# Kernel optimization log

Measured on AMD Instinct MI355X. Metric: run time of the kernel, lower is better.

## Reference

```python
import jax, jax.numpy as jnp
import numpy as np

# --- configuration constants (from conf) ---
FEAT_H, FEAT_W, STRIDE = 32, 110, 16       # KITTI 512x1760 image, stride 16
B, G, NA = 8, 32, 36                       # batch, max GT per image, anchors per location
NUM_CLASSES = 4                            # len(lbls)+1
FG_T, BG_LO, BG_HI, BEST_T = 0.5, 0.0, 0.5, 0.35
L_CLS, L_2D, L_3D = 1.0, 1.0, 1.0          # cls_2d_lambda, bbox_2d_lambda, bbox_3d_lambda


def _locate_anchors(anchors):
    """Tile anchor templates over the feature grid. Returns boxes [A,4], tracker [A]."""
    sx = (jnp.arange(FEAT_W) * STRIDE).astype(jnp.float32)
    sy = (jnp.arange(FEAT_H) * STRIDE).astype(jnp.float32)
    gx, gy = jnp.meshgrid(sx, sy)                              # [H,W]
    shifts = jnp.stack([gx, gy, gx, gy], -1).reshape(-1, 4)    # [H*W,4]
    boxes = shifts[:, None, :] + anchors[None, :, 0:4]         # [H*W,NA,4]
    tracker = jnp.broadcast_to(jnp.arange(NA), (FEAT_H * FEAT_W, NA))
    return boxes.reshape(-1, 4), tracker.reshape(-1)


def _iou(rois, gts):
    # rois [A,4], gts [G,4] -> IoU [A,G]
    x1 = jnp.maximum(rois[:, None, 0], gts[None, :, 0])
    y1 = jnp.maximum(rois[:, None, 1], gts[None, :, 1])
    x2 = jnp.minimum(rois[:, None, 2], gts[None, :, 2])
    y2 = jnp.minimum(rois[:, None, 3], gts[None, :, 3])
    iw = jnp.clip(x2 - x1 + 1.0, 0.0)
    ih = jnp.clip(y2 - y1 + 1.0, 0.0)
    inter = iw * ih
    ar = (rois[:, 2] - rois[:, 0] + 1.0) * (rois[:, 3] - rois[:, 1] + 1.0)
    ag = (gts[:, 2] - gts[:, 0] + 1.0) * (gts[:, 3] - gts[:, 1] + 1.0)
    return inter / (ar[:, None] + ag[None, :] - inter)


def _smooth_l1(x):
    ax = jnp.abs(x)
    return jnp.where(ax < 1.0, 0.5 * ax * ax, ax - 0.5)


def setup_inputs() -> dict:
    key = jax.random.key(0)
    ks = jax.random.split(key, 10)
    A = FEAT_H * FEAT_W * NA
    cls = jax.random.normal(ks[0], (B, A, NUM_CLASSES), jnp.float32)
    bbox_2d = jax.random.normal(ks[1], (B, A, 4), jnp.float32) * 0.1
    bbox_3d = jax.random.normal(ks[2], (B, A, 7), jnp.float32) * 0.1
    # GT 2D boxes inside a 512x1760 image
    x1 = jax.random.uniform(ks[3], (B, G)) * 1500.0
    y1 = jax.random.uniform(ks[4], (B, G)) * 350.0
    w = 30.0 + jax.random.uniform(ks[5], (B, G)) * 200.0
    h = 30.0 + jax.random.uniform(ks[6], (B, G)) * 130.0
    gt_boxes = jnp.stack([x1, y1, x1 + w - 1.0, y1 + h - 1.0], -1)
    # GT 3D: [cx_proj, cy_proj, z, w3d, h3d, l3d, ry]
    k7, k8, k9 = jax.random.split(ks[7], 3)
    z = 5.0 + jax.random.uniform(k7, (B, G)) * 55.0
    dims = 1.0 + jax.random.uniform(k8, (B, G, 3)) * 3.0
    ry = (jax.random.uniform(k9, (B, G)) - 0.5) * (2.0 * np.pi)
    gt_3d = jnp.concatenate([(x1 + w * 0.5)[..., None], (y1 + h * 0.5)[..., None],
                             z[..., None], dims, ry[..., None]], -1)
    gt_labels = jax.random.randint(ks[8], (B, G), 1, NUM_CLASSES)
    gt_valid = jnp.ones((B, G), bool)
    # anchors: [x1,y1,x2,y2, z, w3d, h3d, l3d, ry] (12 scales x 3 aspect ratios)
    scales = np.array([32.0 * (1.26 ** i) for i in range(12)], np.float32)
    ratios = np.array([0.5, 1.0, 1.5], np.float32)
    aw = np.repeat(scales, 3)
    ah = (scales[:, None] * ratios[None, :]).reshape(-1)
    az = np.linspace(60.0, 5.0, NA).astype(np.float32)
    box = np.stack([-(aw - 1) / 2, -(ah - 1) / 2, (aw - 1) / 2, (ah - 1) / 2], -1)
    a3 = np.tile(np.array([1.6, 1.5, 3.9, 0.0], np.float32), (NA, 1))
    anchors = jnp.asarray(np.concatenate([box, az[:, None], a3], -1), jnp.float32)
    bbox_means = jnp.zeros((1, 11), jnp.float32)
    bbox_stds = jnp.concatenate([jnp.full((1, 4), 0.1, jnp.float32),
                                 jnp.full((1, 7), 0.5, jnp.float32)], -1)
    return {"cls": cls, "bbox_2d": bbox_2d, "bbox_3d": bbox_3d,
            "gt_boxes": gt_boxes, "gt_3d": gt_3d, "gt_labels": gt_labels,
            "gt_valid": gt_valid, "anchors": anchors,
            "bbox_means": bbox_means, "bbox_stds": bbox_stds}


def reference(cls, bbox_2d, bbox_3d, gt_boxes, gt_3d, gt_labels, gt_valid,
              anchors, bbox_means, bbox_stds):
    roi_boxes, tracker = _locate_anchors(anchors)          # [A,4], [A]
    widths = roi_boxes[:, 2] - roi_boxes[:, 0] + 1.0
    heights = roi_boxes[:, 3] - roi_boxes[:, 1] + 1.0
    ctr_x = roi_boxes[:, 0] + 0.5 * widths
    ctr_y = roi_boxes[:, 1] + 0.5 * heights
    src = anchors[tracker]                                 # [A,9] per-roi anchor template
    Gn = gt_boxes.shape[1]

    def assign(gtb, gt3, glbl, gval):
        iou = _iou(roi_boxes, gtb)                         # [A,G]
        iou = jnp.where(gval[None, :], iou, -1.0)
        max_ol = iou.max(1)
        agt = iou.argmax(1)                                # assigned GT per anchor
        fg = max_ol >= FG_T
        # best-anchor-per-gt rule (best_thresh)
        gt_best = iou.max(0)
        ba = iou.argmax(0)
        force = gval & (gt_best >= BEST_T)
        fg = fg.at[ba].max(force)
        agt = agt.at[ba].set(jnp.where(force, jnp.arange(Gn), agt[ba]))
        bg = (~fg) & (max_ol < BG_HI) & (max_ol >= BG_LO)  # rest is ignored
        g = gtb[agt]
        g3 = gt3[agt]
        gw = g[:, 2] - g[:, 0] + 1.0
        gh = g[:, 3] - g[:, 1] + 1.0
        gcx = g[:, 0] + 0.5 * gw
        gcy = g[:, 1] + 0.5 * gh
        t2 = jnp.stack([(gcx - ctr_x) / widths, (gcy - ctr_y) / heights,
                        jnp.log(gw / widths), jnp.log(gh / heights)], -1)
        t3 = jnp.stack([(g3[:, 0] - ctr_x) / widths, (g3[:, 1] - ctr_y) / heights,
                        g3[:, 2] - src[:, 4],
                        jnp.log(g3[:, 3] / src[:, 5]),
                        jnp.log(g3[:, 4] / src[:, 6]),
                        jnp.log(g3[:, 5] / src[:, 7]),
                        g3[:, 6] - src[:, 8]], -1)
        t2 = (t2 - bbox_means[0, 0:4]) / bbox_stds[0, 0:4]
        t3 = (t3 - bbox_means[0, 4:11]) / bbox_stds[0, 4:11]
        lbl = jnp.where(fg, glbl[agt], 0)
        return lbl, fg, bg, t2, t3

    lbl, fg, bg, t2, t3 = jax.vmap(assign)(gt_boxes, gt_3d, gt_labels, gt_valid)
    lbl = jax.lax.stop_gradient(lbl)
    t2 = jax.lax.stop_gradient(t2)
    t3 = jax.lax.stop_gradient(t3)
    active = (fg | bg).astype(cls.dtype)
    fgf = fg.astype(cls.dtype)
    logp = jax.nn.log_softmax(cls, -1)
    ce = -jnp.take_along_axis(logp, lbl[..., None], -1)[..., 0]
    n_act = jnp.maximum(active.sum(), 1.0)
    n_fg = jnp.maximum(fgf.sum(), 1.0)
    loss_cls = (ce * active).sum() / n_act
    loss_2d = (_smooth_l1(bbox_2d - t2).sum(-1) * fgf).sum() / n_fg
    loss_3d = (_smooth_l1(bbox_3d - t3).sum(-1) * fgf).sum() / n_fg
    return L_CLS * loss_cls + L_2D * loss_2d + L_3D * loss_3d
```

## Files before the change

kernel.cpp:

```cpp
#include <hip/hip_runtime.h>

#define FEAT_H 32
#define FEAT_W 110
#define NCELL (FEAT_H * FEAT_W)
#define STRIDEPX 16
#define NB 8
#define NG 32
#define NANC 36
#define NC 4
#define A_TOTAL (NCELL * NANC)

#define CPB 576

#define BLK 512
#define CHK 512
#define NCHK 248
#define G2 512
#define CB (G2 / NB)
#define MAXSLOTS 4

__device__ __forceinline__ float smooth_l1(float x) {
    float ax = fabsf(x);
    return ax < 1.f ? 0.5f * ax * ax : ax - 0.5f;
}



__global__ __launch_bounds__(CPB) void k_colpass(
    const float* __restrict__ gt_boxes, const int* __restrict__ gt_valid,
    const float* __restrict__ anchors, unsigned long long* __restrict__ colpart,
    float* __restrict__ acc, unsigned* __restrict__ done) {
#pragma clang fp contract(off)
    __shared__ unsigned long long cand[NANC];
    const int tid = threadIdx.x;
    const int bg = blockIdx.x;
    if (bg == 0) {
        if (tid < 8) acc[tid] = 0.f;
        if (tid == 8) *done = 0u;
    }
    const int t = tid >> 4;
    const int lane = tid & 15;
    const int valid = gt_valid[bg];
    const float g0 = gt_boxes[bg * 4 + 0], g1 = gt_boxes[bg * 4 + 1];
    const float g2 = gt_boxes[bg * 4 + 2], g3 = gt_boxes[bg * 4 + 3];
    const float ag = (g2 - g0 + 1.f) * (g3 - g1 + 1.f);
    const float* ap = anchors + t * 9;
    const float ax0 = ap[0], ay0 = ap[1], ax1 = ap[2], ay1 = ap[3];
    const float aarea = (ax1 - ax0 + 1.f) * (ay1 - ay0 + 1.f);

    float iwm = -1.f; int icol = 0;
    for (int col = lane; col < FEAT_W; col += 16) {
        const float sx = (float)(col * STRIDEPX);
        const float r0 = sx + ax0, r2 = sx + ax1;
        const float xx1 = fmaxf(r0, g0), xx2 = fminf(r2, g2);
        const float iw = fmaxf(xx2 - xx1 + 1.f, 0.f);
        if (iw > iwm) { iwm = iw; icol = col; }
    }
    float ihm = -1.f; int irow = 0;
    for (int row = lane; row < FEAT_H; row += 16) {
        const float sy = (float)(row * STRIDEPX);
        const float r1 = sy + ay0, r3 = sy + ay1;
        const float yy1 = fmaxf(r1, g1), yy2 = fminf(r3, g3);
        const float ih = fmaxf(yy2 - yy1 + 1.f, 0.f);
        if (ih > ihm) { ihm = ih; irow = row; }
    }
    for (int off = 8; off; off >>= 1) {
        const float ow = __shfl_down(iwm, off, 16);
        const int oc = __shfl_down(icol, off, 16);
        if (ow > iwm || (ow == iwm && oc < icol)) { iwm = ow; icol = oc; }
        const float oh = __shfl_down(ihm, off, 16);
        const int orw = __shfl_down(irow, off, 16);
        if (oh > ihm || (oh == ihm && orw < irow)) { ihm = oh; irow = orw; }
    }
    if (lane == 0) {
        const float inter = iwm * ihm;
        const float iou = inter * __builtin_amdgcn_rcpf(aarea + ag - inter);
        const int a = (irow * FEAT_W + icol) * NANC + t;
        cand[t] = valid
            ? (((unsigned long long)__float_as_uint(iou) << 32) |
               (unsigned long long)(0xFFFFFFFFu - (unsigned)a))
            : 0ull;
    }
    __syncthreads();
    if (tid == 0) {
        unsigned long long best = cand[0];
        for (int u = 1; u < NANC; ++u)
            if (cand[u] > best) best = cand[u];
        colpart[bg] = best;
    }
}

__global__ __launch_bounds__(BLK) void k_main(
    const float* __restrict__ cls, const float* __restrict__ bbox_2d,
    const float* __restrict__ bbox_3d, const float* __restrict__ gt_boxes,
    const float* __restrict__ gt_3d, const int* __restrict__ gt_labels,
    const int* __restrict__ gt_valid, const float* __restrict__ anchors,
    const float* __restrict__ means, const float* __restrict__ stds,
    const unsigned long long* __restrict__ colpart, float* __restrict__ acc,
    unsigned* __restrict__ done, float* __restrict__ out) {
#pragma clang fp contract(off)
    __shared__ float ax0_s[NANC], ay0_s[NANC], ax1_s[NANC], ay1_s[NANC];
    __shared__ float anch9[NANC * 9];
    __shared__ float4 gtb4_s[NG];
    __shared__ float ags_s[NG];
    __shared__ float gt3_s[NG * 7];
    __shared__ int lbl_s[NG];
    __shared__ int bag_s[NG], forceg_s[NG];
    __shared__ float mean_s[11], rstd_s[11];
    __shared__ unsigned vmask_s;
    __shared__ float red[5][BLK / 64];
    __shared__ int fixmap[MAXSLOTS * BLK];
    __shared__ unsigned short fglist[MAXSLOTS * BLK];
    __shared__ int nloc;

    const int tid = threadIdx.x;
    const int b = blockIdx.x / CB;
    const int c0 = blockIdx.x % CB;

    for (int i = tid; i < NANC * 9; i += BLK) anch9[i] = anchors[i];
    if (tid < NANC) {
        const float* ap = anchors + tid * 9;
        ax0_s[tid] = ap[0]; ay0_s[tid] = ap[1];
        ax1_s[tid] = ap[2]; ay1_s[tid] = ap[3];
    }
    for (int i = tid; i < NG * 7; i += BLK) gt3_s[i] = gt_3d[b * NG * 7 + i];
    if (tid == 0) nloc = 0;
    int myval = 0;
    if (tid < NG) {
        const float4 q = ((const float4*)gt_boxes)[b * NG + tid];
        gtb4_s[tid] = q;
        ags_s[tid] = (q.z - q.x + 1.f) * (q.w - q.y + 1.f);
        lbl_s[tid] = gt_labels[b * NG + tid];
        myval = gt_valid[b * NG + tid];
        const unsigned long long p = colpart[b * NG + tid];
        const float gbest = __uint_as_float((unsigned)(p >> 32));
        bag_s[tid] = myval ? (int)(0xFFFFFFFFu - (unsigned)(p & 0xFFFFFFFFull)) : 0;
        forceg_s[tid] = (myval && gbest >= 0.35f) ? 1 : 0;
    }
    unsigned long long bal = __ballot(tid < NG && myval);
    if (tid == 0) vmask_s = (unsigned)bal;
    if (tid < 11) { mean_s[tid] = means[tid]; rstd_s[tid] = 1.0f / stds[tid]; }
    for (int i = tid; i < MAXSLOTS * BLK; i += BLK) fixmap[i] = -1;
    __syncthreads();
    if (tid == 0) {
        for (int g = 0; g < NG; ++g) {
            const int ba = bag_s[g];
            const int cb = ba >> 9;
            if (cb % CB == c0) {
                const int k = (cb - c0) / CB;
                const int idx = k * BLK + (ba & (CHK - 1));
                const int e = fixmap[idx];
                const int anyf = ((e >= 0) ? (e & 0x40000000) : 0) |
                                 (forceg_s[g] ? 0x40000000 : 0);
                const int code = forceg_s[g] ? g : 32;
                fixmap[idx] = anyf | code;
            }
        }
    }
    __syncthreads();
    const unsigned vmask = vmask_s;
    const size_t bbase = (size_t)b * A_TOTAL;

    int araw[MAXSLOTS];
    float4 cv[MAXSLOTS];
    float r0a[MAXSLOTS], r1a[MAXSLOTS], r2a[MAXSLOTS], r3a[MAXSLOTS];
    float ara[MAXSLOTS];
#pragma unroll
    for (int k = 0; k < MAXSLOTS; ++k) {
        araw[k] = (c0 + k * CB) * CHK + tid;
        const int ae = araw[k] < A_TOTAL ? araw[k] : (A_TOTAL - 1);
        cv[k] = *(const float4*)(cls + (bbase + ae) * NC);
        const int t = ae % NANC;
        const int cell = ae / NANC;
        const float sx = (float)((cell % FEAT_W) * STRIDEPX);
        const float sy = (float)((cell / FEAT_W) * STRIDEPX);
        r0a[k] = sx + ax0_s[t]; r1a[k] = sy + ay0_s[t];
        r2a[k] = sx + ax1_s[t]; r3a[k] = sy + ay1_s[t];
        ara[k] = (r2a[k] - r0a[k] + 1.f) * (r3a[k] - r1a[k] + 1.f);
    }

    float m[MAXSLOTS] = {-1.f, -1.f, -1.f, -1.f};
    int iagt[MAXSLOTS] = {0, 0, 0, 0};
#pragma unroll 4
    for (int g = 0; g < NG; ++g) {
        if (!((vmask >> g) & 1u)) continue;
        const float4 q = gtb4_s[g];
        const float agv = ags_s[g];
#pragma unroll
        for (int k = 0; k < MAXSLOTS; ++k) {
            const float xx1 = fmaxf(r0a[k], q.x), yy1 = fmaxf(r1a[k], q.y);
            const float xx2 = fminf(r2a[k], q.z), yy2 = fminf(r3a[k], q.w);
            const float iw = fmaxf(xx2 - xx1 + 1.f, 0.f);
            const float ih = fmaxf(yy2 - yy1 + 1.f, 0.f);
            const float inter = iw * ih;
            const float iou = inter * __builtin_amdgcn_rcpf(ara[k] + agv - inter);
            if (iou > m[k]) { m[k] = iou; iagt[k] = g; }
        }
    }

    float sum_ce = 0.f, sum_act = 0.f, sum_fg = 0.f, sum_2d = 0.f, sum_3d = 0.f;
#pragma unroll
    for (int k = 0; k < MAXSLOTS; ++k) {
        const bool live = araw[k] < A_TOTAL;
        const float best = m[k];
        int agt = iagt[k];
        bool fg = best >= 0.5f;
        const int f = fixmap[k * BLK + tid];
        if (f >= 0) {
            if (f & 0x40000000) fg = true;
            const int code = f & 63;
            agt = (code == 32) ? agt : code;
        }
        if (!live) fg = false;
        const bool bgm = live && (!fg) && (best < 0.5f) && (best >= 0.0f);
        const float active = (fg || bgm) ? 1.f : 0.f;
        const int lbl = fg ? lbl_s[agt] : 0;

        const float4 c4 = cv[k];
        const float mx = fmaxf(fmaxf(c4.x, c4.y), fmaxf(c4.z, c4.w));
        const float se = __expf(c4.x - mx) + __expf(c4.y - mx) +
                         __expf(c4.z - mx) + __expf(c4.w - mx);
        const float lse = mx + __logf(se);
        const float csel = (lbl == 0) ? c4.x : (lbl == 1) ? c4.y
                         : (lbl == 2) ? c4.z : c4.w;
        sum_ce += (lse - csel) * active;
        sum_act += active;

        if (fg) {
            sum_fg += 1.f;
            const int p = atomicAdd(&nloc, 1);
            fglist[p] = (unsigned short)((k << 14) | (tid << 5) | agt);
        }
    }

    __syncthreads();
    const int nfgl = nloc;
    for (int i = tid; i < nfgl; i += BLK) {
        const unsigned e = fglist[i];
        const int k2 = (int)(e >> 14);
        const int tid2 = (int)((e >> 5) & 511u);
        const int agt = (int)(e & 31u);
        const int a = (c0 + k2 * CB) * CHK + tid2;
        const int t = a % NANC;
        const int cell = a / NANC;
        const float sx = (float)((cell % FEAT_W) * STRIDEPX);
        const float sy = (float)((cell / FEAT_W) * STRIDEPX);
        const float r0 = sx + ax0_s[t], r1 = sy + ay0_s[t];
        const float r2 = sx + ax1_s[t], r3 = sy + ay1_s[t];
        const float w = r2 - r0 + 1.f, h = r3 - r1 + 1.f;
        const float rw = __builtin_amdgcn_rcpf(w);
        const float rh = __builtin_amdgcn_rcpf(h);
        const float cx = r0 + 0.5f * w, cy = r1 + 0.5f * h;
        const float4 Gq = gtb4_s[agt];
        const float gw = Gq.z - Gq.x + 1.f, gh = Gq.w - Gq.y + 1.f;
        const float gcx = Gq.x + 0.5f * gw, gcy = Gq.y + 0.5f * gh;
        float tt2[4];
        tt2[0] = (gcx - cx) * rw;
        tt2[1] = (gcy - cy) * rh;
        tt2[2] = __logf(gw * rw);
        tt2[3] = __logf(gh * rh);
        const float4 b2 = *(const float4*)(bbox_2d + (bbase + a) * 4);
        const float b2v[4] = {b2.x, b2.y, b2.z, b2.w};
        float l2 = 0.f;
        for (int j = 0; j < 4; ++j)
            l2 += smooth_l1(b2v[j] - (tt2[j] - mean_s[j]) * rstd_s[j]);
        sum_2d += l2;
        const float* q3p = &gt3_s[agt * 7];
        const float* b3 = bbox_3d + (bbase + a) * 7;
        float tt3[7];
        tt3[0] = (q3p[0] - cx) * rw;
        tt3[1] = (q3p[1] - cy) * rh;
        tt3[2] = q3p[2] - anch9[t * 9 + 4];
        tt3[3] = __logf(q3p[3] * __builtin_amdgcn_rcpf(anch9[t * 9 + 5]));
        tt3[4] = __logf(q3p[4] * __builtin_amdgcn_rcpf(anch9[t * 9 + 6]));
        tt3[5] = __logf(q3p[5] * __builtin_amdgcn_rcpf(anch9[t * 9 + 7]));
        tt3[6] = q3p[6] - anch9[t * 9 + 8];
        float l3 = 0.f;
        for (int j = 0; j < 7; ++j)
            l3 += smooth_l1(b3[j] - (tt3[j] - mean_s[4 + j]) * rstd_s[4 + j]);
        sum_3d += l3;
    }

    float vals[5] = {sum_ce, sum_act, sum_fg, sum_2d, sum_3d};
#pragma unroll
    for (int j = 0; j < 5; ++j) {
        float v = vals[j];
        for (int off = 32; off; off >>= 1) v += __shfl_down(v, off, 64);
        if ((tid & 63) == 0) red[j][tid >> 6] = v;
    }
    __syncthreads();
    if (tid == 0) {
        for (int j = 0; j < 5; ++j) {
            float s = 0.f;
            for (int w = 0; w < BLK / 64; ++w) s += red[j][w];
            atomicAdd(&acc[j], s);
        }
        __threadfence();
        const unsigned old = atomicAdd(done, 1u);
        if (old == G2 - 1) {
            const float a0 = atomicAdd(&acc[0], 0.f);
            const float a1 = atomicAdd(&acc[1], 0.f);
            const float a2 = atomicAdd(&acc[2], 0.f);
            const float a3 = atomicAdd(&acc[3], 0.f);
            const float a4 = atomicAdd(&acc[4], 0.f);
            const float nact = fmaxf(a1, 1.f);
            const float nfg = fmaxf(a2, 1.f);
            out[0] = a0 / nact + a3 / nfg + a4 / nfg;
        }
    }
}

extern "C" void kernel_launch(void* const* d_in, const int* in_sizes, int n_in,
                              void* d_out, int out_size, void* d_ws, size_t ws_size,
                              hipStream_t stream) {
    const float* cls      = (const float*)d_in[0];
    const float* bbox_2d  = (const float*)d_in[1];
    const float* bbox_3d  = (const float*)d_in[2];
    const float* gt_boxes = (const float*)d_in[3];
    const float* gt_3d    = (const float*)d_in[4];
    const int*   gt_labels= (const int*)d_in[5];
    const int*   gt_valid = (const int*)d_in[6];
    const float* anchors  = (const float*)d_in[7];
    const float* means    = (const float*)d_in[8];
    const float* stds     = (const float*)d_in[9];

    unsigned long long* colpart = (unsigned long long*)d_ws;
    float* acc = (float*)((char*)d_ws + 8192);
    unsigned* done = (unsigned*)((char*)d_ws + 8192 + 32);
    float* out = (float*)d_out;

    k_colpass<<<NB * NG, CPB, 0, stream>>>(gt_boxes, gt_valid, anchors,
                                           colpart, acc, done);
    k_main<<<G2, BLK, 0, stream>>>(cls, bbox_2d, bbox_3d, gt_boxes, gt_3d,
                                   gt_labels, gt_valid, anchors, means, stds,
                                   colpart, acc, done, out);
}
```

Measured before the change: 158.2 us.

## Double per-thread anchor slots, halve grid, read GT boxes from global in IoU loop

Halves the main-kernel grid and doubles the number of anchor slots each thread handles, so each GT box fetch is reused across eight anchors. The IoU loop now reads GT boxes from global memory with a one-ahead prefetch and computes GT areas inline, and invalid GTs are masked with a select instead of a branch. The cls logits load is moved after the IoU loop to shorten register live ranges. In exchange the kernel uses more registers and launches fewer blocks, which may reduce occupancy and parallelism, and the fglist entries are widened to 32 bits to fit the larger slot index.

Result: faster. 149.8 us (-5.3%).

```diff
diff --git a/kernel.cpp b/kernel.cpp
--- a/kernel.cpp
+++ b/kernel.cpp
@@ -15,9 +15,9 @@
 #define BLK 512
 #define CHK 512
 #define NCHK 248
-#define G2 512
+#define G2 256
 #define CB (G2 / NB)
-#define MAXSLOTS 4
+#define MAXSLOTS 8
 
 __device__ __forceinline__ float smooth_l1(float x) {
     float ax = fabsf(x);
@@ -102,7 +102,6 @@
     __shared__ float ax0_s[NANC], ay0_s[NANC], ax1_s[NANC], ay1_s[NANC];
     __shared__ float anch9[NANC * 9];
     __shared__ float4 gtb4_s[NG];
-    __shared__ float ags_s[NG];
     __shared__ float gt3_s[NG * 7];
     __shared__ int lbl_s[NG];
     __shared__ int bag_s[NG], forceg_s[NG];
@@ -110,7 +109,7 @@
     __shared__ unsigned vmask_s;
     __shared__ float red[5][BLK / 64];
     __shared__ int fixmap[MAXSLOTS * BLK];
-    __shared__ unsigned short fglist[MAXSLOTS * BLK];
+    __shared__ unsigned fglist[MAXSLOTS * BLK];
     __shared__ int nloc;
 
     const int tid = threadIdx.x;
@@ -129,7 +128,6 @@
     if (tid < NG) {
         const float4 q = ((const float4*)gt_boxes)[b * NG + tid];
         gtb4_s[tid] = q;
-        ags_s[tid] = (q.z - q.x + 1.f) * (q.w - q.y + 1.f);
         lbl_s[tid] = gt_labels[b * NG + tid];
         myval = gt_valid[b * NG + tid];
         const unsigned long long p = colpart[b * NG + tid];
@@ -161,15 +159,12 @@
     const unsigned vmask = vmask_s;
     const size_t bbase = (size_t)b * A_TOTAL;
 
-    int araw[MAXSLOTS];
-    float4 cv[MAXSLOTS];
     float r0a[MAXSLOTS], r1a[MAXSLOTS], r2a[MAXSLOTS], r3a[MAXSLOTS];
     float ara[MAXSLOTS];
 #pragma unroll
     for (int k = 0; k < MAXSLOTS; ++k) {
-        araw[k] = (c0 + k * CB) * CHK + tid;
-        const int ae = araw[k] < A_TOTAL ? araw[k] : (A_TOTAL - 1);
-        cv[k] = *(const float4*)(cls + (bbase + ae) * NC);
+        const int araw = (c0 + k * CB) * CHK + tid;
+        const int ae = araw < A_TOTAL ? araw : (A_TOTAL - 1);
         const int t = ae % NANC;
         const int cell = ae / NANC;
         const float sx = (float)((cell % FEAT_W) * STRIDEPX);
@@ -179,13 +174,18 @@
         ara[k] = (r2a[k] - r0a[k] + 1.f) * (r3a[k] - r1a[k] + 1.f);
     }
 
-    float m[MAXSLOTS] = {-1.f, -1.f, -1.f, -1.f};
-    int iagt[MAXSLOTS] = {0, 0, 0, 0};
+    const float4* gtb = (const float4*)gt_boxes + (size_t)b * NG;
+    float m[MAXSLOTS];
+    int ia[MAXSLOTS];
+#pragma unroll
+    for (int k = 0; k < MAXSLOTS; ++k) { m[k] = -1.f; ia[k] = 0; }
+    float4 qn = gtb[0];
 #pragma unroll 4
     for (int g = 0; g < NG; ++g) {
-        if (!((vmask >> g) & 1u)) continue;
-        const float4 q = gtb4_s[g];
-        const float agv = ags_s[g];
+        const float4 q = qn;
+        if (g + 1 < NG) qn = gtb[g + 1];
+        const bool gv = (vmask >> g) & 1u;
+        const float agv = (q.z - q.x + 1.f) * (q.w - q.y + 1.f);
 #pragma unroll
         for (int k = 0; k < MAXSLOTS; ++k) {
             const float xx1 = fmaxf(r0a[k], q.x), yy1 = fmaxf(r1a[k], q.y);
@@ -193,17 +193,25 @@
             const float iw = fmaxf(xx2 - xx1 + 1.f, 0.f);
             const float ih = fmaxf(yy2 - yy1 + 1.f, 0.f);
             const float inter = iw * ih;
-            const float iou = inter * __builtin_amdgcn_rcpf(ara[k] + agv - inter);
-            if (iou > m[k]) { m[k] = iou; iagt[k] = g; }
-        }
-    }
-
+            float iou = inter * __builtin_amdgcn_rcpf(ara[k] + agv - inter);
+            iou = gv ? iou : -1.0f;
+            if (iou > m[k]) { m[k] = iou; ia[k] = g; }
+        }
+    }
+
+    float4 cvk[MAXSLOTS];
+#pragma unroll
+    for (int k = 0; k < MAXSLOTS; ++k) {
+        const int araw = (c0 + k * CB) * CHK + tid;
+        const int ae = araw < A_TOTAL ? araw : (A_TOTAL - 1);
+        cvk[k] = *(const float4*)(cls + (bbase + ae) * NC);
+    }
     float sum_ce = 0.f, sum_act = 0.f, sum_fg = 0.f, sum_2d = 0.f, sum_3d = 0.f;
 #pragma unroll
     for (int k = 0; k < MAXSLOTS; ++k) {
-        const bool live = araw[k] < A_TOTAL;
+        const bool live = ((c0 + k * CB) * CHK + tid) < A_TOTAL;
         const float best = m[k];
-        int agt = iagt[k];
+        int agt = ia[k];
         bool fg = best >= 0.5f;
         const int f = fixmap[k * BLK + tid];
         if (f >= 0) {
@@ -216,7 +224,7 @@
         const float active = (fg || bgm) ? 1.f : 0.f;
         const int lbl = fg ? lbl_s[agt] : 0;
 
-        const float4 c4 = cv[k];
+        const float4 c4 = cvk[k];
         const float mx = fmaxf(fmaxf(c4.x, c4.y), fmaxf(c4.z, c4.w));
         const float se = __expf(c4.x - mx) + __expf(c4.y - mx) +
                          __expf(c4.z - mx) + __expf(c4.w - mx);
@@ -229,7 +237,7 @@
         if (fg) {
             sum_fg += 1.f;
             const int p = atomicAdd(&nloc, 1);
-            fglist[p] = (unsigned short)((k << 14) | (tid << 5) | agt);
+            fglist[p] = ((unsigned)k << 14) | ((unsigned)tid << 5) | (unsigned)agt;
         }
     }
 
```
